# Performance work log

Measured on AMD Instinct MI355X. Metric: run time of the kernel, lower is better.

The kernel has to match this reference:

```python
import jax, jax.numpy as jnp
import numpy as np

N = 50000      # nodes
E = 800000     # edges
IN = 256       # in_channels
OUT = 128      # out_channels
HID = 2 * OUT  # hidden = 2*out_channels


def setup_inputs() -> dict:
    key = jax.random.key(0)
    ks = jax.random.split(key, 8)
    x = jax.random.normal(ks[0], (N, IN), dtype=jnp.float32)
    edge_index = jax.random.randint(ks[1], (2, E), 0, N, dtype=jnp.int32)
    def glorot(k, fan_in, fan_out):
        return jax.random.normal(k, (fan_in, fan_out), jnp.float32) * np.float32(1.0 / np.sqrt(fan_in))
    W1 = glorot(ks[2], IN, HID)
    b1 = jnp.zeros((HID,), jnp.float32)
    Wmu = glorot(ks[3], HID, OUT)
    bmu = jnp.zeros((OUT,), jnp.float32)
    Wls = glorot(ks[4], HID, OUT)
    bls = jnp.zeros((OUT,), jnp.float32)
    return {"x": x, "edge_index": edge_index, "W1": W1, "b1": b1,
            "Wmu": Wmu, "bmu": bmu, "Wls": Wls, "bls": bls}


def reference(x, edge_index, W1, b1, Wmu, bmu, Wls, bls):
    n = x.shape[0]
    # add self-loops (PyG GCNConv default add_self_loops=True)
    loop = jnp.arange(n, dtype=edge_index.dtype)
    src = jnp.concatenate([edge_index[0], loop])  # message sources (row)
    dst = jnp.concatenate([edge_index[1], loop])  # aggregation targets (col)
    # symmetric normalization: deg over targets, norm = d^-1/2[src] * d^-1/2[dst]
    deg = jax.ops.segment_sum(jnp.ones(src.shape[0], x.dtype), dst, num_segments=n)
    dinv = jnp.where(deg > 0, jax.lax.rsqrt(deg), 0.0)
    norm = dinv[src] * dinv[dst]  # [E+N]

    def gcn(h, W, b):
        h = h @ W                                   # [N, F_out] dense transform
        msg = h[src] * norm[:, None]                # gather + scale   [E+N, F_out]
        agg = jax.ops.segment_sum(msg, dst, num_segments=n)  # scatter-add
        return agg + b

    h = jax.nn.relu(gcn(x, W1, b1))
    return gcn(h, Wmu, bmu), gcn(h, Wls, bls)
```

## Files before the change

### kernel.cpp

```cpp
#include <hip/hip_runtime.h>
#include <hip/hip_fp16.h>

typedef __attribute__((ext_vector_type(8))) _Float16 half8;
typedef __attribute__((ext_vector_type(4))) _Float16 half4;
typedef __attribute__((ext_vector_type(4))) float float4v;

#define LDP2 72


__global__ __launch_bounds__(256) void k_deg(const int* __restrict__ dst, int* __restrict__ deg, int E) {
    int e = blockIdx.x * 256 + threadIdx.x;
    if (e < E) atomicAdd(&deg[dst[e]], 1);
}


__global__ __launch_bounds__(256) void k_scan1(const int* __restrict__ deg, int* __restrict__ rowptr,
                                               int* __restrict__ bsum, float* __restrict__ dinv, int N) {
    __shared__ int sm[256];
    const int t = threadIdx.x;
    const int i = blockIdx.x * 256 + t;
    int v = (i < N) ? deg[i] : 0;
    if (i < N) dinv[i] = rsqrtf((float)(v + 1));
    int x = v;
    sm[t] = x;
    __syncthreads();
#pragma unroll
    for (int off = 1; off < 256; off <<= 1) {
        int y = (t >= off) ? sm[t - off] : 0;
        __syncthreads();
        x += y;
        sm[t] = x;
        __syncthreads();
    }
    if (i < N) rowptr[i] = x - v;
    if (t == 255) bsum[blockIdx.x] = x;
}

__global__ __launch_bounds__(256) void k_scan2(int* __restrict__ bsum, int* __restrict__ rowptr, int nb, int N) {
    __shared__ int sm[256];
    const int t = threadIdx.x;
    int v = (t < nb) ? bsum[t] : 0;
    int x = v;
    sm[t] = x;
    __syncthreads();
#pragma unroll
    for (int off = 1; off < 256; off <<= 1) {
        int y = (t >= off) ? sm[t - off] : 0;
        __syncthreads();
        x += y;
        sm[t] = x;
        __syncthreads();
    }
    if (t < nb) bsum[t] = x - v;
    if (t == 255) rowptr[N] = x;
}

__global__ __launch_bounds__(256) void k_scan3(int* __restrict__ rowptr, const int* __restrict__ bsum, int N) {
    int i = blockIdx.x * 256 + threadIdx.x;
    if (i < N) rowptr[i] += bsum[blockIdx.x];
}

__global__ __launch_bounds__(256) void k_fill(const int* __restrict__ src, const int* __restrict__ dst,
                                              const int* __restrict__ rowptr, int* __restrict__ rowcnt,
                                              int* __restrict__ csr, int E) {
    int e = blockIdx.x * 256 + threadIdx.x;
    if (e < E) {
        int d = dst[e];
        int pos = rowptr[d] + atomicAdd(&rowcnt[d], 1);
        csr[pos] = src[e];
    }
}

__global__ __launch_bounds__(256) void k_wt(const float* __restrict__ W1, const float* __restrict__ Wmu,
                                            const float* __restrict__ Wls, _Float16* __restrict__ Wt1,
                                            _Float16* __restrict__ Wct) {
    int b = blockIdx.x;
    int t = threadIdx.x;
    if (b < 256) {
        Wt1[b * 256 + t] = (_Float16)W1[t * 256 + b];
    } else {
        int j = b - 256;
        float v = (j < 128) ? Wmu[t * 128 + j] : Wls[t * 128 + (j - 128)];
        Wct[j * 256 + t] = (_Float16)v;
    }
}

template <int AF32, int OUTF32>
__global__ __launch_bounds__(256) void gemm_k(const void* __restrict__ Aptr, const _Float16* __restrict__ Bt,
                                              const float* __restrict__ bmu, const float* __restrict__ bls,
                                              const float* __restrict__ dinv,
                                              void* __restrict__ outp, int M, size_t split) {
    __shared__ _Float16 As[128 * LDP2];
    __shared__ _Float16 Bs[128 * LDP2];
    const int t = threadIdx.x;
    const int lane = t & 63;
    const int wid = t >> 6;

    const int nwg = gridDim.x;
    const int wg = blockIdx.x;
    const int q8 = nwg >> 3, r8 = nwg & 7;
    const int xcd = wg & 7, pos = wg >> 3;
    const int v = (xcd < r8) ? (xcd * (q8 + 1) + pos) : (r8 * (q8 + 1) + (xcd - r8) * q8 + pos);
    const int bm = (v >> 1) * 128;
    const int bn = (v & 1) * 128;

    const int wm = (wid & 1) * 64;
    const int wn = (wid >> 1) * 64;

    float4v acc[4][4];
#pragma unroll
    for (int i = 0; i < 4; i++)
#pragma unroll
        for (int j = 0; j < 4; j++) acc[i][j] = (float4v){0.f, 0.f, 0.f, 0.f};

    float4v ar32[8];
    half8 ar16[4];
    half8 br[4];

    const int a32row = t >> 1;
    const int a32ko = (t & 1) * 32;

    auto load_regs = [&](int kt) {
        if (AF32) {
            const float* A = (const float*)Aptr;
            int gr = bm + a32row; if (gr >= M) gr = M - 1;
            const float4v* p = (const float4v*)(A + (size_t)gr * 256 + kt + a32ko);
#pragma unroll
            for (int q = 0; q < 8; q++) ar32[q] = p[q];
        } else {
            const _Float16* A = (const _Float16*)Aptr;
#pragma unroll
            for (int m = 0; m < 4; m++) {
                int u = m * 256 + t;
                int row = u >> 3, k8 = (u & 7) * 8;
                int gr = bm + row; if (gr >= M) gr = M - 1;
                int k = kt + k8;
                ar16[m] = *(const half8*)(A + (size_t)(k >> 5) * M * 32 + (size_t)gr * 32 + (k & 31));
            }
        }
#pragma unroll
        for (int m = 0; m < 4; m++) {
            int u = m * 256 + t;
            int row = u >> 3, k8 = (u & 7) * 8;
            br[m] = *(const half8*)(Bt + (size_t)(bn + row) * 256 + kt + k8);
        }
    };

    auto write_lds = [&]() {
        if (AF32) {
#pragma unroll
            for (int q = 0; q < 4; q++) {
                half8 h;
#pragma unroll
                for (int j = 0; j < 4; j++) { h[j] = (_Float16)ar32[2 * q][j]; h[4 + j] = (_Float16)ar32[2 * q + 1][j]; }
                *(half8*)&As[a32row * LDP2 + a32ko + q * 8] = h;
            }
        } else {
#pragma unroll
            for (int m = 0; m < 4; m++) {
                int u = m * 256 + t;
                int row = u >> 3, k8 = (u & 7) * 8;
                *(half8*)&As[row * LDP2 + k8] = ar16[m];
            }
        }
#pragma unroll
        for (int m = 0; m < 4; m++) {
            int u = m * 256 + t;
            int row = u >> 3, k8 = (u & 7) * 8;
            *(half8*)&Bs[row * LDP2 + k8] = br[m];
        }
    };

    load_regs(0);
#pragma unroll
    for (int it = 0; it < 4; it++) {
        if (it > 0) __syncthreads();
        write_lds();
        __syncthreads();
        if (it < 3) load_regs((it + 1) * 64);

        const int kg = (lane >> 4) * 8;
        const int fr = lane & 15;
#pragma unroll
        for (int kk = 0; kk < 64; kk += 32) {
            half8 af[4], bf[4];
#pragma unroll
            for (int f = 0; f < 4; f++) af[f] = *(const half8*)&As[(wm + f * 16 + fr) * LDP2 + kk + kg];
#pragma unroll
            for (int f = 0; f < 4; f++) bf[f] = *(const half8*)&Bs[(wn + f * 16 + fr) * LDP2 + kk + kg];
#pragma unroll
            for (int i = 0; i < 4; i++)
#pragma unroll
                for (int j = 0; j < 4; j++)
                    acc[i][j] = __builtin_amdgcn_mfma_f32_16x16x32_f16(af[i], bf[j], acc[i][j], 0, 0, 0);
        }
    }

    const int fc = lane & 15;
    const int rq = (lane >> 4) * 4;
    if (OUTF32) {
        float* out = (float*)outp;
#pragma unroll
        for (int i = 0; i < 4; i++) {
#pragma unroll
            for (int j = 0; j < 4; j++) {
                int col = bn + wn + j * 16 + fc;
                float bias = (col < 128) ? bmu[col] : bls[col - 128];
#pragma unroll
                for (int r = 0; r < 4; r++) {
                    int row = bm + wm + i * 16 + rq + r;
                    if (row < M) {
                        size_t o = (col < 128) ? ((size_t)row * 128 + col)
                                               : (split + (size_t)row * 128 + (col - 128));
                        out[o] = acc[i][j][r] + bias;
                    }
                }
            }
        }
    } else {
        _Float16* out = (_Float16*)outp;
#pragma unroll
        for (int i = 0; i < 4; i++) {
#pragma unroll
            for (int r = 0; r < 4; r++) {
                int row = bm + wm + i * 16 + rq + r;
                if (row < M) {
                    float sc = dinv[row];
#pragma unroll
                    for (int j = 0; j < 4; j++) {
                        int col = bn + wn + j * 16 + fc;
                        out[(size_t)(col >> 5) * M * 32 + (size_t)row * 32 + (col & 31)] =
                            (_Float16)(acc[i][j][r] * sc);
                    }
                }
            }
        }
    }
}

template <int MODE>
__global__ __launch_bounds__(256) void k_agg_t(const _Float16* __restrict__ in, _Float16* __restrict__ out,
                                               const float* __restrict__ dinv, const int* __restrict__ rowptr,
                                               const int* __restrict__ csr, const float* __restrict__ bias,
                                               int N) {
    const int tile = blockIdx.x & 7;
    const int g = (blockIdx.x >> 3) * 64 + (threadIdx.x >> 2);
    if (g >= N) return;
    const int fq = threadIdx.x & 3;
    const _Float16* __restrict__ tin = in + (size_t)tile * N * 32 + fq * 8;

    const int beg = rowptr[g], end = rowptr[g + 1];

    float acc[8];
    {
        half8 sv = *(const half8*)(tin + (size_t)g * 32);
#pragma unroll
        for (int j = 0; j < 8; j++) acc[j] = (float)sv[j];
    }
#pragma unroll 4
    for (int e = beg; e < end; ++e) {
        int s = csr[e];
        half8 v = *(const half8*)(tin + (size_t)s * 32);
#pragma unroll
        for (int j = 0; j < 8; j++) acc[j] += (float)v[j];
    }

    const float dd = dinv[g];
    half8 o;
    if (MODE) {
        const float4v* bp = (const float4v*)(bias + tile * 32 + fq * 8);
        float4v b0 = bp[0], b1 = bp[1];
#pragma unroll
        for (int j = 0; j < 4; j++) {
            o[j] = (_Float16)(fmaxf(acc[j] * dd + b0[j], 0.f) * dd);
            o[4 + j] = (_Float16)(fmaxf(acc[4 + j] * dd + b1[j], 0.f) * dd);
        }
    } else {
#pragma unroll
        for (int j = 0; j < 8; j++) o[j] = (_Float16)(acc[j] * dd);
    }
    *(half8*)(out + (size_t)tile * N * 32 + (size_t)g * 32 + fq * 8) = o;
}


extern "C" void kernel_launch(void* const* d_in, const int* in_sizes, int n_in,
                              void* d_out, int out_size, void* d_ws, size_t ws_size,
                              hipStream_t stream) {
    const float* x   = (const float*)d_in[0];
    const int*   ei  = (const int*)d_in[1];
    const float* W1  = (const float*)d_in[2];
    const float* b1  = (const float*)d_in[3];
    const float* Wmu = (const float*)d_in[4];
    const float* bmu = (const float*)d_in[5];
    const float* Wls = (const float*)d_in[6];
    const float* bls = (const float*)d_in[7];
    const int N = in_sizes[0] / 256;
    const int E = in_sizes[1] / 2;
    const int* esrc = ei;
    const int* edst = ei + E;

    char* ws = (char*)d_ws;
    size_t off = 0;
    auto alloc = [&](size_t bytes) -> void* {
        void* p = ws + off;
        off += (bytes + 255) & ~(size_t)255;
        return p;
    };
    _Float16* h1  = (_Float16*)alloc((size_t)N * 256 * 2);
    _Float16* hb  = (_Float16*)alloc((size_t)N * 256 * 2);
    _Float16* Wt1 = (_Float16*)alloc(256 * 256 * 2);
    _Float16* Wct = (_Float16*)alloc(256 * 256 * 2);
    float* dinv   = (float*)alloc((size_t)N * 4);
    int* degcnt   = (int*)alloc((size_t)N * 2 * 4);
    int* deg      = degcnt;
    int* rowcnt   = degcnt + N;
    int* rowptr   = (int*)alloc((size_t)(N + 1) * 4);
    int* bsum     = (int*)alloc(256 * 4);
    int* csr      = (int*)alloc((size_t)E * 4);

    const int nb = (N + 255) / 256;

    hipMemsetAsync(degcnt, 0, (size_t)N * 2 * 4, stream);

    k_deg<<<(E + 255) / 256, 256, 0, stream>>>(edst, deg, E);
    k_scan1<<<nb, 256, 0, stream>>>(deg, rowptr, bsum, dinv, N);
    k_scan2<<<1, 256, 0, stream>>>(bsum, rowptr, nb, N);
    k_scan3<<<nb, 256, 0, stream>>>(rowptr, bsum, N);
    k_fill<<<(E + 255) / 256, 256, 0, stream>>>(esrc, edst, rowptr, rowcnt, csr, E);
    k_wt<<<512, 256, 0, stream>>>(W1, Wmu, Wls, Wt1, Wct);

    const int nbm = (N + 127) / 128;
    const int nba = 8 * ((N + 63) / 64);
    gemm_k<1, 0><<<nbm * 2, 256, 0, stream>>>(x, Wt1, nullptr, nullptr, dinv, h1, N, 0);
    k_agg_t<1><<<nba, 256, 0, stream>>>(h1, hb, dinv, rowptr, csr, b1, N);
    k_agg_t<0><<<nba, 256, 0, stream>>>(hb, h1, dinv, rowptr, csr, nullptr, N);
    gemm_k<0, 1><<<nbm * 2, 256, 0, stream>>>(h1, Wct, bmu, bls, nullptr, d_out, N, (size_t)N * 128);
}
```

Measured before the change: 342.2 us.

## Partition CSR fill by destination range and software-pipeline neighbor gathers

The CSR fill kernel now launches eight times as many blocks, and each block handles only edges whose destination falls in one eighth of the node range. The goal is to localize atomics and scattered writes so they hit L2/cache better, at the cost of reading dst eight times. The aggregation kernel now processes neighbors in groups of four with explicit double-buffered register prefetch, keeping more gathers in flight while the previous group is accumulated. This raises register pressure.

```diff
diff --git a/kernel.cpp b/kernel.cpp
--- a/kernel.cpp
+++ b/kernel.cpp
@@ -7,10 +7,24 @@
 
 #define LDP2 72
 
-
 __global__ __launch_bounds__(256) void k_deg(const int* __restrict__ dst, int* __restrict__ deg, int E) {
     int e = blockIdx.x * 256 + threadIdx.x;
     if (e < E) atomicAdd(&deg[dst[e]], 1);
+}
+
+__global__ __launch_bounds__(256) void k_fill(const int* __restrict__ src, const int* __restrict__ dst,
+                                              const int* __restrict__ rowptr, int* __restrict__ rowcnt,
+                                              int* __restrict__ csr, int E, int N) {
+    const int part = blockIdx.x & 7;
+    const int e = (blockIdx.x >> 3) * 256 + threadIdx.x;
+    if (e >= E) return;
+    const int lo = (int)(((long long)part * N) >> 3);
+    const int hi = (int)(((long long)(part + 1) * N) >> 3);
+    int d = dst[e];
+    if (d >= lo && d < hi) {
+        int pos = rowptr[d] + atomicAdd(&rowcnt[d], 1);
+        csr[pos] = src[e];
+    }
 }
 
 
@@ -58,17 +72,6 @@
 __global__ __launch_bounds__(256) void k_scan3(int* __restrict__ rowptr, const int* __restrict__ bsum, int N) {
     int i = blockIdx.x * 256 + threadIdx.x;
     if (i < N) rowptr[i] += bsum[blockIdx.x];
-}
-
-__global__ __launch_bounds__(256) void k_fill(const int* __restrict__ src, const int* __restrict__ dst,
-                                              const int* __restrict__ rowptr, int* __restrict__ rowcnt,
-                                              int* __restrict__ csr, int E) {
-    int e = blockIdx.x * 256 + threadIdx.x;
-    if (e < E) {
-        int d = dst[e];
-        int pos = rowptr[d] + atomicAdd(&rowcnt[d], 1);
-        csr[pos] = src[e];
-    }
 }
 
 __global__ __launch_bounds__(256) void k_wt(const float* __restrict__ W1, const float* __restrict__ Wmu,
@@ -250,6 +253,7 @@
     const _Float16* __restrict__ tin = in + (size_t)tile * N * 32 + fq * 8;
 
     const int beg = rowptr[g], end = rowptr[g + 1];
+    const int nb4 = (end - beg) >> 2;
 
     float acc[8];
     {
@@ -257,8 +261,35 @@
 #pragma unroll
         for (int j = 0; j < 8; j++) acc[j] = (float)sv[j];
     }
-#pragma unroll 4
-    for (int e = beg; e < end; ++e) {
+
+    int e = beg;
+    half8 r0, r1, r2, r3;
+    if (nb4 > 0) {
+        int i0 = csr[e], i1 = csr[e + 1], i2 = csr[e + 2], i3 = csr[e + 3];
+        r0 = *(const half8*)(tin + (size_t)i0 * 32);
+        r1 = *(const half8*)(tin + (size_t)i1 * 32);
+        r2 = *(const half8*)(tin + (size_t)i2 * 32);
+        r3 = *(const half8*)(tin + (size_t)i3 * 32);
+    }
+    for (int b = 0; b + 1 < nb4; ++b) {
+        int n0 = csr[e + 4], n1 = csr[e + 5], n2 = csr[e + 6], n3 = csr[e + 7];
+        half8 s0 = *(const half8*)(tin + (size_t)n0 * 32);
+        half8 s1 = *(const half8*)(tin + (size_t)n1 * 32);
+        half8 s2 = *(const half8*)(tin + (size_t)n2 * 32);
+        half8 s3 = *(const half8*)(tin + (size_t)n3 * 32);
+#pragma unroll
+        for (int j = 0; j < 8; j++)
+            acc[j] += (float)r0[j] + (float)r1[j] + (float)r2[j] + (float)r3[j];
+        r0 = s0; r1 = s1; r2 = s2; r3 = s3;
+        e += 4;
+    }
+    if (nb4 > 0) {
+#pragma unroll
+        for (int j = 0; j < 8; j++)
+            acc[j] += (float)r0[j] + (float)r1[j] + (float)r2[j] + (float)r3[j];
+        e += 4;
+    }
+    for (; e < end; ++e) {
         int s = csr[e];
         half8 v = *(const half8*)(tin + (size_t)s * 32);
 #pragma unroll
@@ -326,7 +357,8 @@
     k_scan1<<<nb, 256, 0, stream>>>(deg, rowptr, bsum, dinv, N);
     k_scan2<<<1, 256, 0, stream>>>(bsum, rowptr, nb, N);
     k_scan3<<<nb, 256, 0, stream>>>(rowptr, bsum, N);
-    k_fill<<<(E + 255) / 256, 256, 0, stream>>>(esrc, edst, rowptr, rowcnt, csr, E);
+    const int nbe = 8 * ((E + 255) / 256);
+    k_fill<<<nbe, 256, 0, stream>>>(esrc, edst, rowptr, rowcnt, csr, E, N);
     k_wt<<<512, 256, 0, stream>>>(W1, Wmu, Wls, Wt1, Wct);
 
     const int nbm = (N + 127) / 128;
```

New measurement: 330.2 us. 1.04x faster.
